# Performance work log

Hardware: AMD Instinct MI355X
Metric: run time of the kernel (lower is better)

Reference implementation:

```python
import jax, jax.numpy as jnp
import numpy as np

T = 131072          # total characters across all words/sentences
N_WORDS = 32768
WORD_DIM = 1024
CHAR_DIM = 256
HIDDEN = 512
NUM_EMB = 40


def setup_inputs() -> dict:
    key = jax.random.key(0)
    ks = jax.random.split(key, 9)
    return {
        "word_emb": jax.random.normal(ks[0], (N_WORDS, WORD_DIM), jnp.float32),
        "char_ids": jax.random.randint(ks[1], (T,), 0, NUM_EMB, jnp.int32),
        "word_ids": jax.random.randint(ks[2], (T,), 0, N_WORDS, jnp.int32),
        "E": jax.random.normal(ks[3], (NUM_EMB, CHAR_DIM), jnp.float32),
        "W_ih": jax.random.normal(ks[4], (4 * HIDDEN, CHAR_DIM), jnp.float32) * 0.05,
        "b_ih": jax.random.normal(ks[5], (4 * HIDDEN,), jnp.float32) * 0.05,
        "b_hh": jax.random.normal(ks[6], (4 * HIDDEN,), jnp.float32) * 0.05,
        "W_lin": jax.random.normal(ks[7], (WORD_DIM, WORD_DIM + HIDDEN), jnp.float32) * 0.02,
        "b_lin": jax.random.normal(ks[8], (WORD_DIM,), jnp.float32) * 0.02,
    }


def reference(word_emb, char_ids, word_ids, E, W_ih, b_ih, b_hh, W_lin, b_lin):
    # Per-char embedding lookup: [T, CHAR_DIM]
    x = E[char_ids]
    # Single LSTM cell step from zero state (source runs LSTM with seq_len=1,
    # batch=num_chars; h0=c0=0 so W_hh @ h0 vanishes and only b_hh remains).
    gates = x @ W_ih.T + b_ih + b_hh            # [T, 4H], torch gate order i,f,g,o
    i, f, g, o = jnp.split(gates, 4, axis=-1)
    c = jax.nn.sigmoid(i) * jnp.tanh(g)          # f * c0 = 0
    h = jax.nn.sigmoid(o) * jnp.tanh(c)          # [T, HIDDEN]
    # Broadcast each word's embedding to its characters (torch .expand())
    we = word_emb[word_ids]                      # [T, WORD_DIM]
    combined = jnp.concatenate([we, h], axis=-1) # [T, WORD_DIM + HIDDEN]
    return jax.nn.relu(combined @ W_lin.T + b_lin)  # [T, WORD_DIM]
```

## Files before the change

### kernel.cpp

```cpp
#include <hip/hip_runtime.h>
#include <cstdint>
#include <cstddef>

#define T_TOTAL   131072
#define NWORDS    32768
#define WDIM      1024
#define CDIM      256
#define HID       512
#define NEMB      40
#define KDIM      1024
#define NDIM      1024

#define BM 128
#define BN 128
#define BK 32
#define NK (KDIM / BK)
#define EPS 132

#define NCONVB_BLKS (NDIM * KDIM / 4 / 256)
#define NCONVA_BLKS (NWORDS * KDIM / 4 / 256)

typedef __attribute__((ext_vector_type(8))) short bf16x8;
typedef __attribute__((ext_vector_type(4))) float f32x4;
typedef __attribute__((ext_vector_type(4))) unsigned short u16x4;

__device__ __forceinline__ unsigned short f2bf(float x) {
  union { float f; unsigned int u; } v; v.f = x;
  unsigned int r = v.u + 0x7fffu + ((v.u >> 16) & 1u);
  return (unsigned short)(r >> 16);
}
__device__ __forceinline__ float bf2f(unsigned short b) {
  union { float f; unsigned int u; } v; v.u = ((unsigned int)b) << 16;
  return v.f;
}

__device__ __forceinline__ void gld16(const void* src, void* lds) {
  __builtin_amdgcn_global_load_lds(
      (const __attribute__((address_space(1))) unsigned int*)src,
      (__attribute__((address_space(3))) unsigned int*)lds, 16, 0, 0);
}

template <bool DO_A>
__global__ __launch_bounds__(256) void k_prep(
    const float* __restrict__ word_emb, const float* __restrict__ E,
    const float* __restrict__ W_ih, const float* __restrict__ b_ih,
    const float* __restrict__ b_hh, const float* __restrict__ W_lin,
    const float* __restrict__ b_lin,
    unsigned short* __restrict__ Ah, unsigned short* __restrict__ Al,
    unsigned short* __restrict__ Bh, unsigned short* __restrict__ Bl,
    float* __restrict__ Hc) {
  __shared__ float sx[CDIM];
  __shared__ float sh[HID];
  int b = blockIdx.x;
  int tid = threadIdx.x;

  if (b < NEMB) {
    int e = b;
    sx[tid] = E[e * CDIM + tid];
    __syncthreads();
    const float4* xv = (const float4*)sx;
#pragma unroll
    for (int rep = 0; rep < 2; ++rep) {
      int j = rep * 256 + tid;
      float si = b_ih[j] + b_hh[j];
      float sg = b_ih[1024 + j] + b_hh[1024 + j];
      float so = b_ih[1536 + j] + b_hh[1536 + j];
      const float4* wi = (const float4*)&W_ih[(size_t)j * CDIM];
      const float4* wg = (const float4*)&W_ih[(size_t)(1024 + j) * CDIM];
      const float4* wo = (const float4*)&W_ih[(size_t)(1536 + j) * CDIM];
      for (int k = 0; k < CDIM / 4; ++k) {
        float4 d = xv[k];
        float4 a = wi[k]; si += a.x*d.x + a.y*d.y + a.z*d.z + a.w*d.w;
        float4 g = wg[k]; sg += g.x*d.x + g.y*d.y + g.z*d.z + g.w*d.w;
        float4 c = wo[k]; so += c.x*d.x + c.y*d.y + c.z*d.z + c.w*d.w;
      }
      float iv = 1.f / (1.f + expf(-si));
      float cv = iv * tanhf(sg);
      float ov = 1.f / (1.f + expf(-so));
      sh[j] = ov * tanhf(cv);
    }
    __syncthreads();
    const float4* hv = (const float4*)sh;
#pragma unroll
    for (int rep = 0; rep < 4; ++rep) {
      int n = rep * 256 + tid;
      float s = b_lin[n];
      const float4* wl = (const float4*)&W_lin[(size_t)n * 1536 + 1024];
      for (int k = 0; k < HID / 4; ++k) {
        float4 a = wl[k], d = hv[k];
        s += a.x*d.x + a.y*d.y + a.z*d.z + a.w*d.w;
      }
      Hc[e * NDIM + n] = s;
    }
    return;
  }
  b -= NEMB;
  if (b < NCONVB_BLKS) {
    long idx = ((long)b * 256 + tid) * 4;
    long r = idx >> 10;
    int c = (int)(idx & 1023);
    const float4 v = *(const float4*)&W_lin[r * 1536 + c];
    unsigned short h0 = f2bf(v.x), h1 = f2bf(v.y), h2 = f2bf(v.z), h3 = f2bf(v.w);
    u16x4 H = {h0, h1, h2, h3};
    u16x4 L = {f2bf(v.x - bf2f(h0)), f2bf(v.y - bf2f(h1)),
               f2bf(v.z - bf2f(h2)), f2bf(v.w - bf2f(h3))};
    *(u16x4*)&Bh[idx] = H;
    *(u16x4*)&Bl[idx] = L;
    return;
  }
  if (DO_A) {
    b -= NCONVB_BLKS;
    long idx = ((long)b * 256 + tid) * 4;
    const float4 v = *(const float4*)&word_emb[idx];
    unsigned short h0 = f2bf(v.x), h1 = f2bf(v.y), h2 = f2bf(v.z), h3 = f2bf(v.w);
    u16x4 H = {h0, h1, h2, h3};
    u16x4 L = {f2bf(v.x - bf2f(h0)), f2bf(v.y - bf2f(h1)),
               f2bf(v.z - bf2f(h2)), f2bf(v.w - bf2f(h3))};
    *(u16x4*)&Ah[idx] = H;
    *(u16x4*)&Al[idx] = L;
  }
}

template <bool PRECONV>
__global__ __launch_bounds__(256, 2) void k_gemm_p(
    const float* __restrict__ Af,
    const unsigned short* __restrict__ Ah, const unsigned short* __restrict__ Al,
    const unsigned short* __restrict__ Bh, const unsigned short* __restrict__ Bl,
    float* __restrict__ P) {
  __shared__ __align__(16) char smem[65536];

  int nwg = gridDim.x;
  int bid = blockIdx.x;
  int cpx = nwg >> 3;
  int swz = (bid & 7) * cpx + (bid >> 3);
  int bn = swz & 7;
  int bm = swz >> 3;

  int tid = threadIdx.x;
  int lane = tid & 63;
  int w = tid >> 6;
  int wr = w >> 1, wc = w & 1;
  int fr = lane & 15, fq = lane >> 4;

  size_t arow0 = (size_t)bm * BM;
  size_t brow0 = (size_t)bn * BN;

  f32x4 acc[4][4];
#pragma unroll
  for (int i = 0; i < 4; ++i)
#pragma unroll
    for (int j = 0; j < 4; ++j) acc[i][j] = (f32x4)0.0f;

  int bOff[4];
#pragma unroll
  for (int ni = 0; ni < 4; ++ni) {
    int row = wc * 64 + ni * 16 + fr;
    bOff[ni] = row * 64 + ((fq ^ ((row >> 1) & 3)) << 4);
  }
  size_t bS[2]; int bL[2];
#pragma unroll
  for (int is = 0; is < 2; ++is) {
    int off = is * 4096 + tid * 16;
    int r = off >> 6;
    int sp = (off >> 4) & 3;
    int colE = ((sp ^ ((r >> 1) & 3)) << 3);
    bS[is] = (brow0 + r) * KDIM + colE;
    bL[is] = is * 4096 + w * 1024;
  }

  if (PRECONV) {
    size_t aS[2];
#pragma unroll
    for (int is = 0; is < 2; ++is) {
      int off = is * 4096 + tid * 16;
      int r = off >> 6;
      int sp = (off >> 4) & 3;
      int colE = ((sp ^ ((r >> 1) & 3)) << 3);
      aS[is] = (arow0 + r) * KDIM + colE;
    }
    int aOff[4];
#pragma unroll
    for (int mi = 0; mi < 4; ++mi) {
      int row = wr * 64 + mi * 16 + fr;
      aOff[mi] = row * 64 + ((fq ^ ((row >> 1) & 3)) << 4);
    }

    auto STAGE = [&](int buf, int k0) {
      char* b = smem + buf * 32768;
#pragma unroll
      for (int is = 0; is < 2; ++is) {
        gld16(Ah + aS[is] + k0, b + bL[is]);
        gld16(Al + aS[is] + k0, b + 8192 + bL[is]);
        gld16(Bh + bS[is] + k0, b + 16384 + bL[is]);
        gld16(Bl + bS[is] + k0, b + 24576 + bL[is]);
      }
    };

    STAGE(0, 0);
    for (int t = 0; t < NK; ++t) {
      char* bufc = smem + (t & 1) * 32768;
      if (t + 1 < NK) {
        STAGE((t + 1) & 1, (t + 1) * BK);
        asm volatile("s_waitcnt vmcnt(8)" ::: "memory");
      } else {
        asm volatile("s_waitcnt vmcnt(0)" ::: "memory");
      }
      __builtin_amdgcn_s_barrier();
      __builtin_amdgcn_sched_barrier(0);

      bf16x8 fah[4], fal[4], fbh[4], fbl[4];
#pragma unroll
      for (int ni = 0; ni < 4; ++ni) {
        fbh[ni] = *(const bf16x8*)(bufc + 16384 + bOff[ni]);
        fbl[ni] = *(const bf16x8*)(bufc + 24576 + bOff[ni]);
      }
#pragma unroll
      for (int mi = 0; mi < 4; ++mi) {
        fah[mi] = *(const bf16x8*)(bufc + aOff[mi]);
        fal[mi] = *(const bf16x8*)(bufc + 8192 + aOff[mi]);
      }
      __builtin_amdgcn_s_setprio(1);
#pragma unroll
      for (int mi = 0; mi < 4; ++mi)
#pragma unroll
        for (int ni = 0; ni < 4; ++ni) {
          acc[mi][ni] = __builtin_amdgcn_mfma_f32_16x16x32_bf16(fah[mi], fbh[ni], acc[mi][ni], 0, 0, 0);
          acc[mi][ni] = __builtin_amdgcn_mfma_f32_16x16x32_bf16(fah[mi], fbl[ni], acc[mi][ni], 0, 0, 0);
          acc[mi][ni] = __builtin_amdgcn_mfma_f32_16x16x32_bf16(fal[mi], fbh[ni], acc[mi][ni], 0, 0, 0);
        }
      __builtin_amdgcn_s_setprio(0);
      __builtin_amdgcn_sched_barrier(0);
      __builtin_amdgcn_s_barrier();
    }
  } else {
    size_t aS[4]; int aL[4];
#pragma unroll
    for (int is = 0; is < 4; ++is) {
      int off = is * 4096 + tid * 16;
      int r = off >> 7;
      int sl = (off >> 4) & 7;
      int col = ((sl ^ (r & 7)) << 2);
      aS[is] = (arow0 + r) * KDIM + col;
      aL[is] = is * 4096 + w * 1024;
    }
    int a1[4], a2[4];
#pragma unroll
    for (int mi = 0; mi < 4; ++mi) {
      int row = wr * 64 + mi * 16 + fr;
      a1[mi] = row * 128 + (((fq << 1)     ^ (row & 7)) << 4);
      a2[mi] = row * 128 + (((fq << 1) + 1) ^ (row & 7)) * 16;
    }

    auto STAGE = [&](int buf, int k0) {
      char* b = smem + buf * 32768;
#pragma unroll
      for (int is = 0; is < 4; ++is) gld16(Af + aS[is] + k0, b + aL[is]);
#pragma unroll
      for (int is = 0; is < 2; ++is) {
        gld16(Bh + bS[is] + k0, b + 16384 + bL[is]);
        gld16(Bl + bS[is] + k0, b + 24576 + bL[is]);
      }
    };

    STAGE(0, 0);
    for (int t = 0; t < NK; ++t) {
      char* bufc = smem + (t & 1) * 32768;
      if (t + 1 < NK) {
        STAGE((t + 1) & 1, (t + 1) * BK);
        asm volatile("s_waitcnt vmcnt(8)" ::: "memory");
      } else {
        asm volatile("s_waitcnt vmcnt(0)" ::: "memory");
      }
      __builtin_amdgcn_s_barrier();
      __builtin_amdgcn_sched_barrier(0);

      bf16x8 fah[4], fal[4], fbh[4], fbl[4];
#pragma unroll
      for (int ni = 0; ni < 4; ++ni) {
        fbh[ni] = *(const bf16x8*)(bufc + 16384 + bOff[ni]);
        fbl[ni] = *(const bf16x8*)(bufc + 24576 + bOff[ni]);
      }
#pragma unroll
      for (int mi = 0; mi < 4; ++mi) {
        float4 v1 = *(const float4*)(bufc + a1[mi]);
        float4 v2 = *(const float4*)(bufc + a2[mi]);
        float f[8] = {v1.x, v1.y, v1.z, v1.w, v2.x, v2.y, v2.z, v2.w};
        union { bf16x8 v; unsigned short u[8]; } H, L;
#pragma unroll
        for (int q = 0; q < 8; ++q) {
          unsigned short hq = f2bf(f[q]);
          H.u[q] = hq;
          L.u[q] = f2bf(f[q] - bf2f(hq));
        }
        fah[mi] = H.v;
        fal[mi] = L.v;
      }
      __builtin_amdgcn_s_setprio(1);
#pragma unroll
      for (int mi = 0; mi < 4; ++mi)
#pragma unroll
        for (int ni = 0; ni < 4; ++ni) {
          acc[mi][ni] = __builtin_amdgcn_mfma_f32_16x16x32_bf16(fah[mi], fbh[ni], acc[mi][ni], 0, 0, 0);
          acc[mi][ni] = __builtin_amdgcn_mfma_f32_16x16x32_bf16(fah[mi], fbl[ni], acc[mi][ni], 0, 0, 0);
          acc[mi][ni] = __builtin_amdgcn_mfma_f32_16x16x32_bf16(fal[mi], fbh[ni], acc[mi][ni], 0, 0, 0);
        }
      __builtin_amdgcn_s_setprio(0);
      __builtin_amdgcn_sched_barrier(0);
      __builtin_amdgcn_s_barrier();
    }
  }

  float* ep = (float*)smem;
  __syncthreads();
#pragma unroll
  for (int half = 0; half < 2; ++half) {
    if (wr == half) {
#pragma unroll
      for (int mi = 0; mi < 4; ++mi)
#pragma unroll
        for (int ni = 0; ni < 4; ++ni)
#pragma unroll
          for (int j = 0; j < 4; ++j) {
            int r = mi * 16 + fq * 4 + j;
            int c = wc * 64 + ni * 16 + fr;
            ep[r * EPS + c] = acc[mi][ni][j];
          }
    }
    __syncthreads();
    for (int i = tid; i < 2048; i += 256) {
      int r = i >> 5;
      int c4 = (i & 31) << 2;
      float4 v = *(const float4*)&ep[r * EPS + c4];
      *(float4*)&P[(arow0 + half * 64 + r) * NDIM + brow0 + c4] = v;
    }
    __syncthreads();
  }
}

__global__ __launch_bounds__(256) void k_out(const int* __restrict__ wid,
                                             const int* __restrict__ cid,
                                             const float* __restrict__ P,
                                             const float* __restrict__ Hc,
                                             float* __restrict__ out) {
  int w = threadIdx.x >> 6, lane = threadIdx.x & 63;
  int t = blockIdx.x * 4 + w;
  int wd = wid[t], cd = cid[t];
  const f32x4* pr = (const f32x4*)&P[(size_t)wd << 10];
  const f32x4* hr = (const f32x4*)&Hc[(size_t)cd << 10];
  f32x4* orow = (f32x4*)&out[(size_t)t << 10];
#pragma unroll
  for (int ch = 0; ch < 4; ++ch) {
    int c = ch * 64 + lane;
    f32x4 a = pr[c];
    f32x4 h4 = hr[c];
    f32x4 r;
    r[0] = fmaxf(a[0] + h4[0], 0.f);
    r[1] = fmaxf(a[1] + h4[1], 0.f);
    r[2] = fmaxf(a[2] + h4[2], 0.f);
    r[3] = fmaxf(a[3] + h4[3], 0.f);
    __builtin_nontemporal_store(r, &orow[c]);
  }
}

extern "C" void kernel_launch(void* const* d_in, const int* in_sizes, int n_in,
                              void* d_out, int out_size, void* d_ws, size_t ws_size,
                              hipStream_t stream) {
  (void)in_sizes; (void)n_in; (void)out_size;
  const float* word_emb = (const float*)d_in[0];
  const int*   char_ids = (const int*)d_in[1];
  const int*   word_ids = (const int*)d_in[2];
  const float* E        = (const float*)d_in[3];
  const float* W_ih     = (const float*)d_in[4];
  const float* b_ih     = (const float*)d_in[5];
  const float* b_hh     = (const float*)d_in[6];
  const float* W_lin    = (const float*)d_in[7];
  const float* b_lin    = (const float*)d_in[8];
  float* out = (float*)d_out;
  char* ws = (char*)d_ws;

  size_t o = 0;
  auto alloc = [&](size_t b) { size_t r = o; o = (o + b + 255) & ~(size_t)255; return r; };
  size_t oHc = alloc((size_t)NEMB * NDIM * 4);
  size_t oBh = alloc((size_t)NDIM * KDIM * 2);
  size_t oBl = alloc((size_t)NDIM * KDIM * 2);
  size_t oP  = alloc((size_t)NWORDS * NDIM * 4);
  size_t szB = o;
  size_t oAh = alloc((size_t)NWORDS * KDIM * 2);
  size_t oAl = alloc((size_t)NWORDS * KDIM * 2);
  size_t szA = o;

  float* Hc          = (float*)(ws + oHc);
  unsigned short* Bh = (unsigned short*)(ws + oBh);
  unsigned short* Bl = (unsigned short*)(ws + oBl);
  float* P           = (float*)(ws + oP);
  unsigned short* Ah = (unsigned short*)(ws + oAh);
  unsigned short* Al = (unsigned short*)(ws + oAl);

  int grid = (NWORDS / BM) * (NDIM / BN);

  if (ws_size >= szA) {
    k_prep<true><<<NEMB + NCONVB_BLKS + NCONVA_BLKS, 256, 0, stream>>>(
        word_emb, E, W_ih, b_ih, b_hh, W_lin, b_lin, Ah, Al, Bh, Bl, Hc);
    k_gemm_p<true><<<grid, 256, 0, stream>>>(word_emb, Ah, Al, Bh, Bl, P);
  } else {
    k_prep<false><<<NEMB + NCONVB_BLKS, 256, 0, stream>>>(
        word_emb, E, W_ih, b_ih, b_hh, W_lin, b_lin, nullptr, nullptr, Bh, Bl, Hc);
    k_gemm_p<false><<<grid, 256, 0, stream>>>(word_emb, nullptr, nullptr, Bh, Bl, P);
  }
  k_out<<<T_TOTAL / 4, 256, 0, stream>>>(word_ids, char_ids, P, Hc, out);
}
```

Before: 481.6 us.

## Use 256x256 tile GEMM with split-bf16 passes as virtual K and triple buffering

Replaces the preconverted 128x128 GEMM with a 512-thread 256x256 tile kernel. The three bf16 product passes (Ah*Bh, Ah*Bl, Al*Bh) are laid out as 96 virtual K steps that each load one A and one B slice, so each pass uses a single MFMA stream. Loads are triple-buffered with a prefetch distance of two, and results are written directly to global memory without the shared-memory epilogue. The aim is more reuse per loaded tile and less global traffic per FLOP, at the cost of higher register pressure (128 accumulators per thread) and uncoalesced direct stores.

```diff
diff --git a/kernel.cpp b/kernel.cpp
--- a/kernel.cpp
+++ b/kernel.cpp
@@ -11,6 +11,10 @@
 #define KDIM      1024
 #define NDIM      1024
 
+#define GBM 256
+#define GBN 256
+#define GBK 32
+#define NKV 96
 #define BM 128
 #define BN 128
 #define BK 32
@@ -121,10 +125,119 @@
   }
 }
 
-template <bool PRECONV>
-__global__ __launch_bounds__(256, 2) void k_gemm_p(
+__global__ __launch_bounds__(512, 2) void k_gemm_p256(
+    const unsigned short* __restrict__ Ah, const unsigned short* __restrict__ Al,
+    const unsigned short* __restrict__ Bh, const unsigned short* __restrict__ Bl,
+    float* __restrict__ P) {
+  __shared__ __align__(16) char smem[98304];
+
+  int bid = blockIdx.x;
+  int swz = (bid & 7) * 64 + (bid >> 3);
+  int bm = swz >> 2;
+  int bn = swz & 3;
+
+  int tid = threadIdx.x;
+  int lane = tid & 63;
+  int w = tid >> 6;
+  int wm = w >> 2, wn = w & 3;
+  int fr = lane & 15, fq = lane >> 4;
+
+  size_t arow0 = (size_t)bm * GBM;
+  size_t brow0 = (size_t)bn * GBN;
+
+  f32x4 acc[8][4];
+#pragma unroll
+  for (int i = 0; i < 8; ++i)
+#pragma unroll
+    for (int j = 0; j < 4; ++j) acc[i][j] = (f32x4)0.0f;
+
+  size_t aS[2], bS[2];
+  int sL[2];
+#pragma unroll
+  for (int is = 0; is < 2; ++is) {
+    int off = is * 8192 + tid * 16;
+    int r = off >> 6;
+    int sp = (off >> 4) & 3;
+    int colE = ((sp ^ ((r >> 1) & 3)) << 3);
+    aS[is] = (arow0 + r) * KDIM + colE;
+    bS[is] = (brow0 + r) * KDIM + colE;
+    sL[is] = is * 8192 + w * 1024;
+  }
+  int aOff[8], bOff[4];
+#pragma unroll
+  for (int mi = 0; mi < 8; ++mi) {
+    int row = wm * 128 + mi * 16 + fr;
+    aOff[mi] = row * 64 + ((fq ^ ((row >> 1) & 3)) << 4);
+  }
+#pragma unroll
+  for (int ni = 0; ni < 4; ++ni) {
+    int row = wn * 64 + ni * 16 + fr;
+    bOff[ni] = row * 64 + ((fq ^ ((row >> 1) & 3)) << 4);
+  }
+
+  auto STAGE = [&](int buf, int vt) {
+    const unsigned short* aB = (vt < 64) ? Ah : Al;
+    const unsigned short* bB = (vt < 32) ? Bh : ((vt < 64) ? Bl : Bh);
+    int k0 = (vt & 31) << 5;
+    char* L = smem + buf * 32768;
+#pragma unroll
+    for (int is = 0; is < 2; ++is) {
+      gld16(aB + aS[is] + k0, L + sL[is]);
+      gld16(bB + bS[is] + k0, L + 16384 + sL[is]);
+    }
+  };
+
+  STAGE(0, 0);
+  STAGE(1, 1);
+  asm volatile("s_waitcnt vmcnt(4)" ::: "memory");
+  __builtin_amdgcn_s_barrier();
+  __builtin_amdgcn_sched_barrier(0);
+
+  for (int t = 0; t < NKV; ++t) {
+    char* bufc = smem + (t % 3) * 32768;
+
+    bf16x8 fah[8], fb[4];
+#pragma unroll
+    for (int ni = 0; ni < 4; ++ni)
+      fb[ni] = *(const bf16x8*)(bufc + 16384 + bOff[ni]);
+#pragma unroll
+    for (int mi = 0; mi < 8; ++mi)
+      fah[mi] = *(const bf16x8*)(bufc + aOff[mi]);
+
+    if (t + 2 < NKV) STAGE((t + 2) % 3, t + 2);
+
+    __builtin_amdgcn_s_setprio(1);
+#pragma unroll
+    for (int mi = 0; mi < 8; ++mi)
+#pragma unroll
+      for (int ni = 0; ni < 4; ++ni)
+        acc[mi][ni] = __builtin_amdgcn_mfma_f32_16x16x32_bf16(fah[mi], fb[ni], acc[mi][ni], 0, 0, 0);
+    __builtin_amdgcn_s_setprio(0);
+    __builtin_amdgcn_sched_barrier(0);
+
+    if (t < NKV - 2) {
+      asm volatile("s_waitcnt vmcnt(4)" ::: "memory");
+    } else {
+      asm volatile("s_waitcnt vmcnt(0)" ::: "memory");
+    }
+    __builtin_amdgcn_s_barrier();
+    __builtin_amdgcn_sched_barrier(0);
+  }
+
+  size_t pbase = (arow0 + wm * 128) * NDIM + brow0 + wn * 64 + fr;
+#pragma unroll
+  for (int mi = 0; mi < 8; ++mi)
+#pragma unroll
+    for (int j = 0; j < 4; ++j) {
+      size_t rowoff = (size_t)(mi * 16 + fq * 4 + j) * NDIM;
+#pragma unroll
+      for (int ni = 0; ni < 4; ++ni)
+        P[pbase + rowoff + ni * 16] = acc[mi][ni][j];
+    }
+}
+
+__global__ __launch_bounds__(256, 2) void k_gemm_p_f32(
     const float* __restrict__ Af,
-    const unsigned short* __restrict__ Ah, const unsigned short* __restrict__ Al,
     const unsigned short* __restrict__ Bh, const unsigned short* __restrict__ Bl,
     float* __restrict__ P) {
   __shared__ __align__(16) char smem[65536];
@@ -167,147 +280,80 @@
     bS[is] = (brow0 + r) * KDIM + colE;
     bL[is] = is * 4096 + w * 1024;
   }
-
-  if (PRECONV) {
-    size_t aS[2];
+  size_t aS[4]; int aL[4];
+#pragma unroll
+  for (int is = 0; is < 4; ++is) {
+    int off = is * 4096 + tid * 16;
+    int r = off >> 7;
+    int sl = (off >> 4) & 7;
+    int col = ((sl ^ (r & 7)) << 2);
+    aS[is] = (arow0 + r) * KDIM + col;
+    aL[is] = is * 4096 + w * 1024;
+  }
+  int a1[4], a2[4];
+#pragma unroll
+  for (int mi = 0; mi < 4; ++mi) {
+    int row = wr * 64 + mi * 16 + fr;
+    a1[mi] = row * 128 + (((fq << 1)     ^ (row & 7)) << 4);
+    a2[mi] = row * 128 + (((fq << 1) + 1) ^ (row & 7)) * 16;
+  }
+
+  auto STAGE = [&](int buf, int k0) {
+    char* b = smem + buf * 32768;
+#pragma unroll
+    for (int is = 0; is < 4; ++is) gld16(Af + aS[is] + k0, b + aL[is]);
 #pragma unroll
     for (int is = 0; is < 2; ++is) {
-      int off = is * 4096 + tid * 16;
-      int r = off >> 6;
-      int sp = (off >> 4) & 3;
-      int colE = ((sp ^ ((r >> 1) & 3)) << 3);
-      aS[is] = (arow0 + r) * KDIM + colE;
-    }
-    int aOff[4];
+      gld16(Bh + bS[is] + k0, b + 16384 + bL[is]);
+      gld16(Bl + bS[is] + k0, b + 24576 + bL[is]);
+    }
+  };
+
+  STAGE(0, 0);
+  for (int t = 0; t < NK; ++t) {
+    char* bufc = smem + (t & 1) * 32768;
+    if (t + 1 < NK) {
+      STAGE((t + 1) & 1, (t + 1) * BK);
+      asm volatile("s_waitcnt vmcnt(8)" ::: "memory");
+    } else {
+      asm volatile("s_waitcnt vmcnt(0)" ::: "memory");
+    }
+    __builtin_amdgcn_s_barrier();
+    __builtin_amdgcn_sched_barrier(0);
+
+    bf16x8 fah[4], fal[4], fbh[4], fbl[4];
+#pragma unroll
+    for (int ni = 0; ni < 4; ++ni) {
+      fbh[ni] = *(const bf16x8*)(bufc + 16384 + bOff[ni]);
+      fbl[ni] = *(const bf16x8*)(bufc + 24576 + bOff[ni]);
+    }
 #pragma unroll
     for (int mi = 0; mi < 4; ++mi) {
-      int row = wr * 64 + mi * 16 + fr;
-      aOff[mi] = row * 64 + ((fq ^ ((row >> 1) & 3)) << 4);
-    }
-
-    auto STAGE = [&](int buf, int k0) {
-      char* b = smem + buf * 32768;
-#pragma unroll
-      for (int is = 0; is < 2; ++is) {
-        gld16(Ah + aS[is] + k0, b + bL[is]);
-        gld16(Al + aS[is] + k0, b + 8192 + bL[is]);
-        gld16(Bh + bS[is] + k0, b + 16384 + bL[is]);
-        gld16(Bl + bS[is] + k0, b + 24576 + bL[is]);
+      float4 v1 = *(const float4*)(bufc + a1[mi]);
+      float4 v2 = *(const float4*)(bufc + a2[mi]);
+      float f[8] = {v1.x, v1.y, v1.z, v1.w, v2.x, v2.y, v2.z, v2.w};
+      union { bf16x8 v; unsigned short u[8]; } H, L;
+#pragma unroll
+      for (int q = 0; q < 8; ++q) {
+        unsigned short hq = f2bf(f[q]);
+        H.u[q] = hq;
+        L.u[q] = f2bf(f[q] - bf2f(hq));
       }
-    };
-
-    STAGE(0, 0);
-    for (int t = 0; t < NK; ++t) {
-      char* bufc = smem + (t & 1) * 32768;
-      if (t + 1 < NK) {
-        STAGE((t + 1) & 1, (t + 1) * BK);
-        asm volatile("s_waitcnt vmcnt(8)" ::: "memory");
-      } else {
-        asm volatile("s_waitcnt vmcnt(0)" ::: "memory");
+      fah[mi] = H.v;
+      fal[mi] = L.v;
+    }
+    __builtin_amdgcn_s_setprio(1);
+#pragma unroll
+    for (int mi = 0; mi < 4; ++mi)
+#pragma unroll
+      for (int ni = 0; ni < 4; ++ni) {
+        acc[mi][ni] = __builtin_amdgcn_mfma_f32_16x16x32_bf16(fah[mi], fbh[ni], acc[mi][ni], 0, 0, 0);
+        acc[mi][ni] = __builtin_amdgcn_mfma_f32_16x16x32_bf16(fah[mi], fbl[ni], acc[mi][ni], 0, 0, 0);
+        acc[mi][ni] = __builtin_amdgcn_mfma_f32_16x16x32_bf16(fal[mi], fbh[ni], acc[mi][ni], 0, 0, 0);
       }
-      __builtin_amdgcn_s_barrier();
-      __builtin_amdgcn_sched_barrier(0);
-
-      bf16x8 fah[4], fal[4], fbh[4], fbl[4];
-#pragma unroll
-      for (int ni = 0; ni < 4; ++ni) {
-        fbh[ni] = *(const bf16x8*)(bufc + 16384 + bOff[ni]);
-        fbl[ni] = *(const bf16x8*)(bufc + 24576 + bOff[ni]);
-      }
-#pragma unroll
-      for (int mi = 0; mi < 4; ++mi) {
-        fah[mi] = *(const bf16x8*)(bufc + aOff[mi]);
-        fal[mi] = *(const bf16x8*)(bufc + 8192 + aOff[mi]);
-      }
-      __builtin_amdgcn_s_setprio(1);
-#pragma unroll
-      for (int mi = 0; mi < 4; ++mi)
-#pragma unroll
-        for (int ni = 0; ni < 4; ++ni) {
-          acc[mi][ni] = __builtin_amdgcn_mfma_f32_16x16x32_bf16(fah[mi], fbh[ni], acc[mi][ni], 0, 0, 0);
-          acc[mi][ni] = __builtin_amdgcn_mfma_f32_16x16x32_bf16(fah[mi], fbl[ni], acc[mi][ni], 0, 0, 0);
-          acc[mi][ni] = __builtin_amdgcn_mfma_f32_16x16x32_bf16(fal[mi], fbh[ni], acc[mi][ni], 0, 0, 0);
-        }
-      __builtin_amdgcn_s_setprio(0);
-      __builtin_amdgcn_sched_barrier(0);
-      __builtin_amdgcn_s_barrier();
-    }
-  } else {
-    size_t aS[4]; int aL[4];
-#pragma unroll
-    for (int is = 0; is < 4; ++is) {
-      int off = is * 4096 + tid * 16;
-      int r = off >> 7;
-      int sl = (off >> 4) & 7;
-      int col = ((sl ^ (r & 7)) << 2);
-      aS[is] = (arow0 + r) * KDIM + col;
-      aL[is] = is * 4096 + w * 1024;
-    }
-    int a1[4], a2[4];
-#pragma unroll
-    for (int mi = 0; mi < 4; ++mi) {
-      int row = wr * 64 + mi * 16 + fr;
-      a1[mi] = row * 128 + (((fq << 1)     ^ (row & 7)) << 4);
-      a2[mi] = row * 128 + (((fq << 1) + 1) ^ (row & 7)) * 16;
-    }
-
-    auto STAGE = [&](int buf, int k0) {
-      char* b = smem + buf * 32768;
-#pragma unroll
-      for (int is = 0; is < 4; ++is) gld16(Af + aS[is] + k0, b + aL[is]);
-#pragma unroll
-      for (int is = 0; is < 2; ++is) {
-        gld16(Bh + bS[is] + k0, b + 16384 + bL[is]);
-        gld16(Bl + bS[is] + k0, b + 24576 + bL[is]);
-      }
-    };
-
-    STAGE(0, 0);
-    for (int t = 0; t < NK; ++t) {
-      char* bufc = smem + (t & 1) * 32768;
-      if (t + 1 < NK) {
-        STAGE((t + 1) & 1, (t + 1) * BK);
-        asm volatile("s_waitcnt vmcnt(8)" ::: "memory");
-      } else {
-        asm volatile("s_waitcnt vmcnt(0)" ::: "memory");
-      }
-      __builtin_amdgcn_s_barrier();
-      __builtin_amdgcn_sched_barrier(0);
-
-      bf16x8 fah[4], fal[4], fbh[4], fbl[4];
-#pragma unroll
-      for (int ni = 0; ni < 4; ++ni) {
-        fbh[ni] = *(const bf16x8*)(bufc + 16384 + bOff[ni]);
-        fbl[ni] = *(const bf16x8*)(bufc + 24576 + bOff[ni]);
-      }
-#pragma unroll
-      for (int mi = 0; mi < 4; ++mi) {
-        float4 v1 = *(const float4*)(bufc + a1[mi]);
-        float4 v2 = *(const float4*)(bufc + a2[mi]);
-        float f[8] = {v1.x, v1.y, v1.z, v1.w, v2.x, v2.y, v2.z, v2.w};
-        union { bf16x8 v; unsigned short u[8]; } H, L;
-#pragma unroll
-        for (int q = 0; q < 8; ++q) {
-          unsigned short hq = f2bf(f[q]);
-          H.u[q] = hq;
-          L.u[q] = f2bf(f[q] - bf2f(hq));
-        }
-        fah[mi] = H.v;
-        fal[mi] = L.v;
-      }
-      __builtin_amdgcn_s_setprio(1);
-#pragma unroll
-      for (int mi = 0; mi < 4; ++mi)
-#pragma unroll
-        for (int ni = 0; ni < 4; ++ni) {
-          acc[mi][ni] = __builtin_amdgcn_mfma_f32_16x16x32_bf16(fah[mi], fbh[ni], acc[mi][ni], 0, 0, 0);
-          acc[mi][ni] = __builtin_amdgcn_mfma_f32_16x16x32_bf16(fah[mi], fbl[ni], acc[mi][ni], 0, 0, 0);
-          acc[mi][ni] = __builtin_amdgcn_mfma_f32_16x16x32_bf16(fal[mi], fbh[ni], acc[mi][ni], 0, 0, 0);
-        }
-      __builtin_amdgcn_s_setprio(0);
-      __builtin_amdgcn_sched_barrier(0);
-      __builtin_amdgcn_s_barrier();
-    }
+    __builtin_amdgcn_s_setprio(0);
+    __builtin_amdgcn_sched_barrier(0);
+    __builtin_amdgcn_s_barrier();
   }
 
   float* ep = (float*)smem;
@@ -396,16 +442,14 @@
   unsigned short* Ah = (unsigned short*)(ws + oAh);
   unsigned short* Al = (unsigned short*)(ws + oAl);
 
-  int grid = (NWORDS / BM) * (NDIM / BN);
-
   if (ws_size >= szA) {
     k_prep<true><<<NEMB + NCONVB_BLKS + NCONVA_BLKS, 256, 0, stream>>>(
         word_emb, E, W_ih, b_ih, b_hh, W_lin, b_lin, Ah, Al, Bh, Bl, Hc);
-    k_gemm_p<true><<<grid, 256, 0, stream>>>(word_emb, Ah, Al, Bh, Bl, P);
+    k_gemm_p256<<<(NWORDS / GBM) * (NDIM / GBN), 512, 0, stream>>>(Ah, Al, Bh, Bl, P);
   } else {
     k_prep<false><<<NEMB + NCONVB_BLKS, 256, 0, stream>>>(
         word_emb, E, W_ih, b_ih, b_hh, W_lin, b_lin, nullptr, nullptr, Bh, Bl, Hc);
-    k_gemm_p<false><<<grid, 256, 0, stream>>>(word_emb, nullptr, nullptr, Bh, Bl, P);
+    k_gemm_p_f32<<<(NWORDS / BM) * (NDIM / BN), 256, 0, stream>>>(word_emb, Bh, Bl, P);
   }
   k_out<<<T_TOTAL / 4, 256, 0, stream>>>(word_ids, char_ids, P, Hc, out);
 }
```

New measurement: 674.6 us. +40.1%, slower.
